# Kernel optimization log

Hardware: AMD Instinct MI355X
Metric: run time of the kernel (lower is better)

Reference implementation:

```python
import jax, jax.numpy as jnp
import numpy as np

B, TIN, E, TOUT, NMEL = 32, 512, 576, 400, 80
PRE, ARNN, DRNN, ADIM, NF, KS = 256, 1024, 1024, 128, 32, 31


def setup_inputs() -> dict:
    key = jax.random.key(0)
    ks = jax.random.split(key, 24)
    r = lambda i, sh, s=0.02: jax.random.normal(ks[i], sh, dtype=jnp.float32) * s
    return {
        'memory': jax.random.normal(ks[0], (B, TIN, E), dtype=jnp.float32) * 0.5,
        'decoder_inputs': jax.random.normal(ks[1], (B, TOUT, NMEL), dtype=jnp.float32) * 0.5,
        'prenet_W1': r(2, (PRE, NMEL)),
        'prenet_W2': r(3, (PRE, PRE)),
        'att_Wih': r(4, (4 * ARNN, PRE + E)),
        'att_Whh': r(5, (4 * ARNN, ARNN)),
        'att_bih': r(6, (4 * ARNN,)),
        'att_bhh': r(7, (4 * ARNN,)),
        'qW': r(8, (ADIM, ARNN)),
        'memW': r(9, (ADIM, E)),
        'convW': r(10, (NF, 2, KS)),
        'convb': r(11, (NF,)),
        'locW': r(12, (ADIM, NF)),
        'vW': r(13, (ADIM,)),
        'dec_Wih': r(14, (4 * DRNN, ARNN + E)),
        'dec_Whh': r(15, (4 * DRNN, DRNN)),
        'dec_bih': r(16, (4 * DRNN,)),
        'dec_bhh': r(17, (4 * DRNN,)),
        'projW': r(18, (NMEL, DRNN + E)),
        'projb': r(19, (NMEL,)),
        'gateW': r(20, (1, DRNN + E)),
        'gateb': r(21, (1,)),
        'memory_lengths': jnp.clip(jax.random.randint(ks[22], (B,), 1, TIN + 1), 16, TIN),
    }


def _lstm(x, h, c, Wih, Whh, bih, bhh):
    g = x @ Wih.T + bih + h @ Whh.T + bhh
    i, f, gg, o = jnp.split(g, 4, axis=-1)  # torch LSTMCell gate order i,f,g,o
    c = jax.nn.sigmoid(f) * c + jax.nn.sigmoid(i) * jnp.tanh(gg)
    h = jax.nn.sigmoid(o) * jnp.tanh(c)
    return h, c


def _forward(memory, decoder_inputs, prenet_W1, prenet_W2, att_Wih, att_Whh, att_bih,
             att_bhh, qW, memW, convW, convb, locW, vW, dec_Wih, dec_Whh, dec_bih,
             dec_bhh, projW, projb, gateW, gateb, memory_lengths):
    b, tin, e = memory.shape
    # go frame + teacher forcing inputs -> prenet (dropout off in deterministic eval)
    go = jnp.zeros((b, 1, NMEL), dtype=memory.dtype)
    di = jnp.concatenate([go, decoder_inputs], axis=1)          # [B, T+1, NMEL]
    x = jax.nn.relu(di @ prenet_W1.T)
    x = jax.nn.relu(x @ prenet_W2.T)                            # [B, T+1, PRE]
    xs = jnp.swapaxes(x, 0, 1)[:-1]                             # [T, B, PRE]
    pmem = memory @ memW.T                                      # [B, TIN, ADIM]
    invalid = jnp.arange(tin)[None, :] >= memory_lengths[:, None]
    pad = KS // 2

    init = (jnp.zeros((b, ARNN)), jnp.zeros((b, ARNN)),
            jnp.zeros((b, DRNN)), jnp.zeros((b, DRNN)),
            jnp.zeros((b, tin)), jnp.zeros((b, tin)),
            jnp.zeros((b, e)))

    def step(carry, xt):
        ah, ac, dh, dc, aw, awc, ctx = carry
        ci = jnp.concatenate([xt, ctx], axis=-1)
        ah, ac = _lstm(ci, ah, ac, att_Wih, att_Whh, att_bih, att_bhh)
        ah = ac  # faithful to source: dropout(attention_cell) overwrites hidden (identity in eval)
        wc = jnp.stack([aw, awc], axis=1)                       # [B, 2, TIN]
        loc = jax.lax.conv_general_dilated(
            wc, convW, (1,), [(pad, pad)],
            dimension_numbers=('NCH', 'OIH', 'NCH')) + convb[None, :, None]
        loc = jnp.swapaxes(loc, 1, 2) @ locW.T                  # [B, TIN, ADIM]
        q = (ah @ qW.T)[:, None, :]                             # [B, 1, ADIM]
        en = jnp.tanh(q + pmem + loc) @ vW                      # [B, TIN]
        en = jnp.where(invalid, -jnp.inf, en)
        aw = jax.nn.softmax(en, axis=1)
        ctx = jnp.einsum('bt,bte->be', aw, memory)
        awc = awc + aw
        d_in = jnp.concatenate([ah, ctx], axis=-1)
        dh, dc = _lstm(d_in, dh, dc, dec_Wih, dec_Whh, dec_bih, dec_bhh)
        dhc = jnp.concatenate([dh, ctx], axis=-1)
        mel = dhc @ projW.T + projb                             # [B, NMEL]
        gate = (dhc @ gateW.T + gateb)[:, 0]                    # [B]
        return (ah, ac, dh, dc, aw, awc, ctx), (mel, gate, aw)

    _, (mels, gates, aligns) = jax.lax.scan(step, init, xs)
    mel_out = jnp.swapaxes(jnp.swapaxes(mels, 0, 1), 1, 2)      # [B, NMEL, T]
    gate_out = jnp.swapaxes(gates, 0, 1)                        # [B, T]
    align_out = jnp.swapaxes(aligns, 0, 1)                      # [B, T, TIN]
    return mel_out, gate_out, align_out


def reference(memory, decoder_inputs, prenet_W1, prenet_W2, att_Wih, att_Whh, att_bih,
              att_bhh, qW, memW, convW, convb, locW, vW, dec_Wih, dec_Whh, dec_bih,
              dec_bhh, projW, projb, gateW, gateb, memory_lengths):
    return _forward(memory, decoder_inputs, prenet_W1, prenet_W2, att_Wih, att_Whh,
                    att_bih, att_bhh, qW, memW, convW, convb, locW, vW, dec_Wih,
                    dec_Whh, dec_bih, dec_bhh, projW, projb, gateW, gateb,
                    memory_lengths)
```

## Files before the change

### kernel.cpp

```cpp
#include <hip/hip_runtime.h>
#include <stdint.h>


#define NB  32
#define TI  512
#define ED  576
#define TO  400
#define NM  80
#define PR  256
#define AR  1024
#define DR  1024
#define AD  128
#define NFl 32
#define KSz 31
#define KA  1856
#define KD  2624
#define NKT_A 58
#define NKT_D 82
#define REL_IDX 320
#define MF_OFF  512

#define SCR_CWB 3584
#define SCR_ACC 4608
#define SCR_DCC 4736
#define SCR_SQ  4864
#define LDS_WA_BYTES (NKT_A*512*2)
#define LDS_WD_BYTES (NKT_D*512*2)
#define LDS_SCR_FLOATS 4992
#define LDS_TOTAL (LDS_WA_BYTES + LDS_WD_BYTES + LDS_SCR_FLOATS*4)

typedef __attribute__((ext_vector_type(8))) short bf8_t;
typedef __attribute__((ext_vector_type(4))) float f4_t;
typedef __attribute__((ext_vector_type(2))) float f2_t;
typedef unsigned long long ull;

__device__ __forceinline__ short f2bf(float f){
  union { float f; unsigned u; } v; v.f = f;
  unsigned r = v.u + 0x7fffu + ((v.u >> 16) & 1u);
  return (short)(r >> 16);
}
__device__ __forceinline__ float bf2f(short s){
  union { unsigned u; float f; } v; v.u = ((unsigned)(unsigned short)s) << 16; return v.f;
}
__device__ __forceinline__ float sigm(float x){ return 1.f / (1.f + __expf(-x)); }

__device__ __forceinline__ f4_t MFMA(bf8_t a, bf8_t b, f4_t c){
  return __builtin_amdgcn_mfma_f32_16x16x32_bf16(a, b, c, 0, 0, 0);
}

__device__ __forceinline__ float cld(const float* p){
  return __hip_atomic_load(p, __ATOMIC_RELAXED, __HIP_MEMORY_SCOPE_AGENT);
}
__device__ __forceinline__ void cst(float* p, float v){
  __hip_atomic_store(p, v, __ATOMIC_RELAXED, __HIP_MEMORY_SCOPE_AGENT);
}
__device__ __forceinline__ ull cld8(const void* p){
  return __hip_atomic_load((const ull*)p, __ATOMIC_RELAXED, __HIP_MEMORY_SCOPE_AGENT);
}
__device__ __forceinline__ void cst8(void* p, ull v){
  __hip_atomic_store((ull*)p, v, __ATOMIC_RELAXED, __HIP_MEMORY_SCOPE_AGENT);
}
__device__ __forceinline__ bf8_t cld_bf8(const short* p){
  union { bf8_t v; ull q[2]; } u;
  u.q[0] = cld8(p); u.q[1] = cld8(p + 4);
  return u.v;
}
__device__ __forceinline__ void cst_bf8(short* p, bf8_t v){
  union { bf8_t v; ull q[2]; } u; u.v = v;
  cst8(p, u.q[0]); cst8(p + 4, u.q[1]);
}

__device__ __forceinline__ bf8_t packrow(const float* p){
  f4_t a = *(const f4_t*)p;
  f4_t b = *(const f4_t*)(p + 4);
  bf8_t r;
  r[0]=f2bf(a[0]); r[1]=f2bf(a[1]); r[2]=f2bf(a[2]); r[3]=f2bf(a[3]);
  r[4]=f2bf(b[0]); r[5]=f2bf(b[1]); r[6]=f2bf(b[2]); r[7]=f2bf(b[3]);
  return r;
}
__device__ __forceinline__ bf8_t packrow_coh(const float* p){
  union { ull q; float f[2]; } u0, u1, u2, u3;
  u0.q = cld8(p); u1.q = cld8(p + 2); u2.q = cld8(p + 4); u3.q = cld8(p + 6);
  bf8_t r;
  r[0]=f2bf(u0.f[0]); r[1]=f2bf(u0.f[1]);
  r[2]=f2bf(u1.f[0]); r[3]=f2bf(u1.f[1]);
  r[4]=f2bf(u2.f[0]); r[5]=f2bf(u2.f[1]);
  r[6]=f2bf(u3.f[0]); r[7]=f2bf(u3.f[1]);
  return r;
}

struct Par {
  const float *X2, *PMEM;
  const short *WA, *WD, *WQ, *WLOC, *MEMBT, *PJW;
  const float *BSA, *BSD;
  const float *convW, *convb, *vW;
  const float *projb, *gateb;
  const int *mlen;
  float *AC, *DH, *CTX, *AW, *AWC, *EN, *QP;
  short *ABA, *ABD;
  float *out_mel, *out_gate, *out_align;
  unsigned *FLAGS;
};

__device__ __forceinline__ const float* aptr_att(const Par& p, int rp, int t, int b, int k){
  if (k < PR)      return p.X2 + ((size_t)t*NB + b)*PR + k;
  if (k < PR+ED)   return p.CTX + (size_t)rp*NB*ED + b*ED + (k - PR);
  return p.AC + (size_t)b*AR + (k - PR - ED);
}

__device__ __forceinline__ void loadD(const Par& p, int cpar, int ks, int lane,
                                      bf8_t& a0, bf8_t& a1){
  if (ks >= 32 && ks < 50){
    const int kb = ks*32 + ((lane >> 4) << 3);
    const float* c0 = p.CTX + (size_t)cpar*NB*ED + (size_t)(lane & 15)*ED + (kb - AR);
    const float* c1 = p.CTX + (size_t)cpar*NB*ED + (size_t)(16 + (lane & 15))*ED + (kb - AR);
    a0 = packrow_coh(c0);
    a1 = packrow_coh(c1);
  } else {
    a0 = cld_bf8(p.ABD + ((size_t)(0*NKT_D + ks)*64 + lane)*8);
    a1 = cld_bf8(p.ABD + ((size_t)(1*NKT_D + ks)*64 + lane)*8);
  }
}

__device__ __forceinline__ void gbar(unsigned* flags, unsigned tgt){
  __syncthreads();
  if (threadIdx.x == 0)
    __hip_atomic_store(&flags[blockIdx.x], tgt, __ATOMIC_RELAXED, __HIP_MEMORY_SCOPE_AGENT);
  if (blockIdx.x == 0){
    if (threadIdx.x < 256){
      while (__hip_atomic_load(&flags[threadIdx.x], __ATOMIC_RELAXED, __HIP_MEMORY_SCOPE_AGENT) < tgt) {}
    }
    __syncthreads();
    if (threadIdx.x == 0)
      __hip_atomic_store(&flags[REL_IDX], tgt, __ATOMIC_RELAXED, __HIP_MEMORY_SCOPE_AGENT);
  }
  if (threadIdx.x == 0){
    while (__hip_atomic_load(&flags[REL_IDX], __ATOMIC_RELAXED, __HIP_MEMORY_SCOPE_AGENT) < tgt) {}
  }
  __syncthreads();
}

__device__ __forceinline__ void sibbar(unsigned* mf, int bid, int tid, unsigned tgt){
  __syncthreads();
  if (tid == 0)
    __hip_atomic_store(&mf[bid], tgt, __ATOMIC_RELAXED, __HIP_MEMORY_SCOPE_AGENT);
  const int g = (bid >> 3) << 3;
  if (tid < 8){
    while (__hip_atomic_load(&mf[g + tid], __ATOMIC_RELAXED, __HIP_MEMORY_SCOPE_AGENT) < tgt) {}
  }
  __syncthreads();
}

__device__ __forceinline__ void reduce8(float* scr, f4_t& a0, f4_t& a1, int lane, int wv){
  if (wv > 0){
    float* slot = scr + (size_t)((wv - 1)*64 + lane)*8;
    *(f4_t*)slot       = a0;
    *(f4_t*)(slot + 4) = a1;
  }
  __syncthreads();
  if (wv == 0){
    #pragma unroll
    for (int w = 0; w < 7; ++w){
      const float* s2 = scr + (size_t)(w*64 + lane)*8;
      a0 += *(const f4_t*)s2;
      a1 += *(const f4_t*)(s2 + 4);
    }
  }
  __syncthreads();
}

__device__ __forceinline__ void dec_gates_cell(const Par& p, const short* sWD, float* scr,
                                               float* sDCc, int cpar, int bid,
                                               int lane, int wv, int tid){
  f4_t acc0 = (f4_t){0.f,0.f,0.f,0.f}, acc1 = (f4_t){0.f,0.f,0.f,0.f};
  {
    bf8_t A0[6], A1[6];
    #pragma unroll
    for (int i = 0; i < 6; ++i) loadD(p, cpar, wv + i*8, lane, A0[i], A1[i]);
    #pragma unroll
    for (int i = 0; i < 6; ++i){
      const bf8_t bw = *((const bf8_t*)sWD + (wv + i*8)*64 + lane);
      acc0 = MFMA(A0[i], bw, acc0);
      acc1 = MFMA(A1[i], bw, acc1);
    }
  }
  {
    bf8_t A0[5], A1[5];
    #pragma unroll
    for (int i = 0; i < 5; ++i){
      const int ks = wv + (i + 6)*8;
      if (ks < NKT_D) loadD(p, cpar, ks, lane, A0[i], A1[i]);
    }
    #pragma unroll
    for (int i = 0; i < 5; ++i){
      const int ks = wv + (i + 6)*8;
      if (ks < NKT_D){
        const bf8_t bw = *((const bf8_t*)sWD + ks*64 + lane);
        acc0 = MFMA(A0[i], bw, acc0);
        acc1 = MFMA(A1[i], bw, acc1);
      }
    }
  }
  reduce8(scr, acc0, acc1, lane, wv);
  float* sG = scr;
  if (wv == 0){
    const int col = lane & 15, rb2 = (lane >> 4) << 2;
    const int jp = (col & 3)*1024 + bid*4 + (col >> 2);
    const float bs = p.BSD[jp];
    #pragma unroll
    for (int r = 0; r < 4; ++r){
      sG[(rb2 + r)*16 + col]      = acc0[r] + bs;
      sG[(16 + rb2 + r)*16 + col] = acc1[r] + bs;
    }
  }
  __syncthreads();
  if (tid < 128){
    const int b = tid >> 2, ul = tid & 3;
    const float gi = sG[b*16 + ul*4 + 0];
    const float gf = sG[b*16 + ul*4 + 1];
    const float gg = sG[b*16 + ul*4 + 2];
    const float go = sG[b*16 + ul*4 + 3];
    const float c  = sigm(gf) * sDCc[tid] + sigm(gi) * tanhf(gg);
    sDCc[tid] = c;
    cst(&p.DH[(size_t)b*DR + bid*4 + ul], sigm(go) * tanhf(c));
  }
  __syncthreads();
}

__device__ void dec_proj(const Par& p, int b, int tprev, int tid, float* sIN){
  const float* ctxg = p.CTX + (size_t)(tprev & 1)*NB*ED + b*ED;
  float h0  = cld(&p.DH[(size_t)b*DR + tid]);
  float h1  = cld(&p.DH[(size_t)b*DR + 512 + tid]);
  float cx0 = cld(ctxg + tid);
  float cx1 = (tid < ED - 512) ? cld(ctxg + 512 + tid) : 0.f;
  sIN[tid] = h0; sIN[512 + tid] = h1;
  sIN[1024 + tid] = cx0;
  if (tid < ED - 512) sIN[1536 + tid] = cx1;
  if (tid < 448) sIN[1600 + tid] = 0.f;
  __syncthreads();
  const int lane = tid & 63, wv = tid >> 6;
  for (int o = wv; o < 81; o += 8){
    const short* wr = p.PJW + (size_t)o*2048 + lane*8;
    float s = 0.f;
    #pragma unroll
    for (int j = 0; j < 4; ++j){
      const bf8_t w8 = *(const bf8_t*)(wr + j*512);
      const float* v = sIN + j*512 + lane*8;
      s += v[0]*bf2f(w8[0]) + v[1]*bf2f(w8[1]) + v[2]*bf2f(w8[2]) + v[3]*bf2f(w8[3])
         + v[4]*bf2f(w8[4]) + v[5]*bf2f(w8[5]) + v[6]*bf2f(w8[6]) + v[7]*bf2f(w8[7]);
    }
    #pragma unroll
    for (int d = 32; d > 0; d >>= 1) s += __shfl_down(s, d);
    if (lane == 0){
      if (o < 80) p.out_mel[((size_t)b*NM + o)*TO + tprev] = s + p.projb[o];
      else        p.out_gate[(size_t)b*TO + tprev] = s + p.gateb[0];
    }
  }
  __syncthreads();
}

__global__ __launch_bounds__(512) void k_loop(Par p){
  const int bid = blockIdx.x, tid = threadIdx.x;
  const int lane = tid & 63, wv = tid >> 6;

  extern __shared__ char dsm[];
  short* sWA = (short*)dsm;
  short* sWD = (short*)(dsm + LDS_WA_BYTES);
  float* scr = (float*)(dsm + LDS_WA_BYTES + LDS_WD_BYTES);
  float* sACc = scr + SCR_ACC;
  float* sDCc = scr + SCR_DCC;
  unsigned* mf = p.FLAGS + MF_OFF;

  {
    if (tid < 128){ sACc[tid] = 0.f; sDCc[tid] = 0.f; }
    const bf8_t* gwa = (const bf8_t*)(p.WA + (size_t)bid*NKT_A*512);
    bf8_t* lwa = (bf8_t*)sWA;
    for (int i = tid; i < NKT_A*64; i += 512) lwa[i] = gwa[i];
    const bf8_t* gwd = (const bf8_t*)(p.WD + (size_t)bid*NKT_D*512);
    bf8_t* lwd = (bf8_t*)sWD;
    for (int i = tid; i < NKT_D*64; i += 512) lwd[i] = gwd[i];
    __syncthreads();
  }

  for (int t = 0; t < TO; ++t){
    const int wp = t & 1, rp = wp ^ 1;
    const unsigned base = (unsigned)(t * 3);

    {
      f4_t acc0 = (f4_t){0.f,0.f,0.f,0.f}, acc1 = (f4_t){0.f,0.f,0.f,0.f};
      bf8_t A0[8], A1[8];
      #pragma unroll
      for (int i = 0; i < 8; ++i){
        const int ks = wv + i*8;
        if (ks < NKT_A){
          if (t == 0 || (ks >= 8 && ks < 26)){
            const int kb = ks*32 + ((lane >> 4) << 3);
            const float* p0 = aptr_att(p, rp, t, lane & 15, kb);
            const float* p1 = aptr_att(p, rp, t, 16 + (lane & 15), kb);
            if (kb < PR){ A0[i] = packrow(p0);     A1[i] = packrow(p1);     }
            else        { A0[i] = packrow_coh(p0); A1[i] = packrow_coh(p1); }
          } else {
            A0[i] = cld_bf8(p.ABA + ((size_t)(0*NKT_A + ks)*64 + lane)*8);
            A1[i] = cld_bf8(p.ABA + ((size_t)(1*NKT_A + ks)*64 + lane)*8);
          }
        }
      }
      #pragma unroll
      for (int i = 0; i < 8; ++i){
        const int ks = wv + i*8;
        if (ks < NKT_A){
          const bf8_t bw = *((const bf8_t*)sWA + ks*64 + lane);
          acc0 = MFMA(A0[i], bw, acc0);
          acc1 = MFMA(A1[i], bw, acc1);
        }
      }
      reduce8(scr, acc0, acc1, lane, wv);
      float* sG = scr;
      if (wv == 0){
        const int col = lane & 15, rb2 = (lane >> 4) << 2;
        const int jp = (col & 3)*1024 + bid*4 + (col >> 2);
        const float bs = p.BSA[jp];
        #pragma unroll
        for (int r = 0; r < 4; ++r){
          sG[(rb2 + r)*16 + col]      = acc0[r] + bs;
          sG[(16 + rb2 + r)*16 + col] = acc1[r] + bs;
        }
      }
      __syncthreads();
      if (tid < 128){
        const int b = tid >> 2, ul = tid & 3;
        const float gi = sG[b*16 + ul*4 + 0];
        const float gf = sG[b*16 + ul*4 + 1];
        const float gg = sG[b*16 + ul*4 + 2];
        const float c  = sigm(gf) * sACc[tid] + sigm(gi) * tanhf(gg);
        sACc[tid] = c;
        cst(&p.AC[(size_t)b*AR + bid*4 + ul], c);
      }
      __syncthreads();
      if (t > 0) dec_gates_cell(p, sWD, scr, sDCc, rp, bid, lane, wv, tid);
      const int b = bid >> 3, tc = bid & 7, t0 = tc*64;
      float* sAWI = scr;
      short* sCwB = (short*)(scr + SCR_CWB);
      for (int i = tid; i < 94; i += 512){
        int g = t0 - 15 + i;
        float a = 0.f, w = 0.f;
        if (g >= 0 && g < TI){
          a = cld(&p.AW [(size_t)rp*NB*TI + b*TI + g]);
          w = cld(&p.AWC[(size_t)rp*NB*TI + b*TI + g]);
        }
        sAWI[2*i] = a; sAWI[2*i + 1] = w;
      }
      __syncthreads();
      {
        const int wvu = __builtin_amdgcn_readfirstlane(wv);
        const int f0 = wvu * 4;
        float ac4[4];
        #pragma unroll
        for (int ff = 0; ff < 4; ++ff) ac4[ff] = p.convb[f0 + ff];
        for (int k = 0; k < KSz; ++k){
          f2_t a2 = *(const f2_t*)&sAWI[2*(lane + k)];
          #pragma unroll
          for (int ff = 0; ff < 4; ++ff){
            ac4[ff] += a2[0] * p.convW[((f0+ff)*2 + 0)*KSz + k]
                     + a2[1] * p.convW[((f0+ff)*2 + 1)*KSz + k];
          }
        }
        #pragma unroll
        for (int ff = 0; ff < 4; ++ff) sCwB[lane*32 + f0 + ff] = f2bf(ac4[ff]);
      }
    }
    gbar(p.FLAGS, base + 1);

    {
      if (bid < 32){
        const int nt = bid >> 2, kc = bid & 3;
        const int kt = kc*8 + wv;
        const int kb = kt*32 + ((lane >> 4) << 3);
        bf8_t a0 = packrow_coh(p.AC + (size_t)(lane & 15)*AR + kb);
        bf8_t a1 = packrow_coh(p.AC + (size_t)(16 + (lane & 15))*AR + kb);
        const bf8_t bw = *(const bf8_t*)(p.WQ + ((size_t)(nt*32 + kt)*64 + lane)*8);
        f4_t q0 = (f4_t){0.f,0.f,0.f,0.f}, q1 = (f4_t){0.f,0.f,0.f,0.f};
        q0 = MFMA(a0, bw, q0);
        q1 = MFMA(a1, bw, q1);
        reduce8(scr, q0, q1, lane, wv);
        if (wv == 0){
          const int col = lane & 15, rb2 = (lane >> 4) << 2;
          float* qp = p.QP + (size_t)kc*NB*AD;
          #pragma unroll
          for (int r = 0; r < 4; ++r){
            cst(&qp[(rb2 + r)*AD + nt*16 + col],      q0[r]);
            cst(&qp[(16 + rb2 + r)*AD + nt*16 + col], q1[r]);
          }
        }
      }
      if (bid >= 224 && t > 0) dec_proj(p, bid - 224, t - 1, tid, scr);
    }
    gbar(p.FLAGS, base + 2);

    {
      float* sQ = scr + SCR_SQ;
      if (tid < 128){
        const int b = bid >> 3;
        sQ[tid] = cld(&p.QP[(size_t)b*AD + tid])
                + cld(&p.QP[(size_t)NB*AD + b*AD + tid])
                + cld(&p.QP[(size_t)2*NB*AD + b*AD + tid])
                + cld(&p.QP[(size_t)3*NB*AD + b*AD + tid]);
      }
      if (wv == 0 && bid < 208){
        const int r = lane & 15, koff = (lane >> 4) << 3;
        if (bid < 80){
          if (t < TO - 1){
            const int m = bid / 40, idx = bid % 40;
            const int ks = (idx < 8) ? idx : idx + 18;
            const int row = m*16 + r;
            const int k = ks*32 + koff;
            bf8_t v = (k < PR)
              ? packrow(p.X2 + ((size_t)(t+1)*NB + row)*PR + k)
              : packrow_coh(p.AC + (size_t)row*AR + (k - PR - ED));
            cst_bf8(p.ABA + ((size_t)(m*NKT_A + ks)*64 + lane)*8, v);
          }
        } else {
          const int j2 = bid - 80;
          const int m = j2 / 64, idx = j2 % 64;
          const int ks = (idx < 32) ? idx : idx + 18;
          const int row = m*16 + r;
          const int k = ks*32 + koff;
          bf8_t v = (k < AR)
            ? packrow_coh(p.AC + (size_t)row*AR + k)
            : packrow_coh(p.DH + (size_t)row*DR + (k - AR - ED));
          cst_bf8(p.ABD + ((size_t)(m*NKT_D + ks)*64 + lane)*8, v);
        }
      }
      __syncthreads();
      const int b = bid >> 3, tc = bid & 7, t0 = tc*64;
      short* sCwB = (short*)(scr + SCR_CWB);
      float* eP = scr;
      const int g = lane >> 4, li = lane & 15;
      const int d2 = wv*16 + li;
      const float vw = p.vW[d2];
      const float qd = sQ[d2];
      const bf8_t bfr = *(const bf8_t*)(p.WLOC + (size_t)(wv*64 + lane)*8);
      #pragma unroll
      for (int mt = 0; mt < 4; ++mt){
        const bf8_t afr = *(const bf8_t*)(sCwB + (mt*16 + li)*32 + (g << 3));
        f4_t c = (f4_t){0.f,0.f,0.f,0.f};
        c = MFMA(afr, bfr, c);
        #pragma unroll
        for (int r = 0; r < 4; ++r){
          const int tg = t0 + mt*16 + g*4 + r;
          const float val = c[r] + p.PMEM[((size_t)b*TI + tg)*AD + d2];
          float v = vw * tanhf(qd + val);
          v += __shfl_xor(v, 1);
          v += __shfl_xor(v, 2);
          v += __shfl_xor(v, 4);
          v += __shfl_xor(v, 8);
          if (li == 0) eP[wv*64 + mt*16 + g*4 + r] = v;
        }
      }
      __syncthreads();
      if (tid < 64){
        float e = eP[tid];
        #pragma unroll
        for (int w2 = 1; w2 < 8; ++w2) e += eP[w2*64 + tid];
        const int tg = t0 + tid;
        cst(&p.EN[b*TI + tg], (tg < p.mlen[b]) ? e : -1e30f);
      }
    }
    sibbar(mf, bid, tid, (unsigned)(t + 1));

    {
      const int b = bid >> 3, ec = bid & 7;
      float* red = scr;
      float* sp  = scr + 64;
      const float e = cld(&p.EN[b*TI + tid]);
      float m = e;
      #pragma unroll
      for (int d = 32; d > 0; d >>= 1) m = fmaxf(m, __shfl_xor(m, d));
      if (lane == 0) red[wv] = m;
      __syncthreads();
      const float M = fmaxf(fmaxf(fmaxf(red[0], red[1]), fmaxf(red[2], red[3])),
                            fmaxf(fmaxf(red[4], red[5]), fmaxf(red[6], red[7])));
      const float x = __expf(e - M);
      float z = x;
      #pragma unroll
      for (int d = 32; d > 0; d >>= 1) z += __shfl_xor(z, d);
      __syncthreads();
      if (lane == 0) red[wv] = z;
      __syncthreads();
      const float Z = red[0]+red[1]+red[2]+red[3]+red[4]+red[5]+red[6]+red[7];
      const float pv = x / Z;
      sp[tid] = pv;
      __syncthreads();
      if (ec == 0){
        cst(&p.AW [(size_t)wp*NB*TI + b*TI + tid], pv);
        cst(&p.AWC[(size_t)wp*NB*TI + b*TI + tid],
            cld(&p.AWC[(size_t)rp*NB*TI + b*TI + tid]) + pv);
        p.out_align[((size_t)b*TO + t)*TI + tid] = pv;
      }
      #pragma unroll
      for (int ii = 0; ii < 9; ++ii){
        const int e2 = ec*72 + wv*9 + ii;
        const short* row = p.MEMBT + ((size_t)b*ED + e2)*TI;
        const bf8_t w8 = *(const bf8_t*)(row + lane*8);
        const float* v = sp + lane*8;
        float a2 = v[0]*bf2f(w8[0]) + v[1]*bf2f(w8[1]) + v[2]*bf2f(w8[2]) + v[3]*bf2f(w8[3])
                 + v[4]*bf2f(w8[4]) + v[5]*bf2f(w8[5]) + v[6]*bf2f(w8[6]) + v[7]*bf2f(w8[7]);
        #pragma unroll
        for (int d = 32; d > 0; d >>= 1) a2 += __shfl_down(a2, d);
        if (lane == 0)
          cst(&p.CTX[(size_t)wp*NB*ED + b*ED + e2], a2);
      }
    }
    gbar(p.FLAGS, base + 3);
  }

  dec_gates_cell(p, sWD, scr, sDCc, (TO - 1) & 1, bid, lane, wv, tid);
  gbar(p.FLAGS, (unsigned)(TO*3 + 1));
  if (bid >= 224) dec_proj(p, bid - 224, TO - 1, tid, scr);
}

__global__ __launch_bounds__(256) void k_init(float* z, int nz,
                                              float* bsa, const float* a1, const float* a2,
                                              float* bsd, const float* d1, const float* d2){
  const int idx = blockIdx.x*256 + threadIdx.x, st = gridDim.x*256;
  const int NG = 4096;
  for (int i = idx; i < nz; i += st) z[i] = 0.f;
  for (int i = idx; i < NG; i += st){ bsa[i] = a1[i] + a2[i]; bsd[i] = d1[i] + d2[i]; }
}

__global__ __launch_bounds__(256) void k_prenet1(const float* di, const float* W1, float* X1){
  const int t = blockIdx.x, tid = threadIdx.x;
  __shared__ float sdi[NB*NM];
  for (int i = tid; i < NB*NM; i += 256){
    const int b = i / NM, k = i - b*NM;
    sdi[i] = (t == 0) ? 0.f : di[((size_t)b*TO + (t-1))*NM + k];
  }
  __syncthreads();
  float acc[NB];
  #pragma unroll
  for (int b = 0; b < NB; ++b) acc[b] = 0.f;
  const int j = tid;
  for (int k = 0; k < NM; ++k){
    const float w = W1[j*NM + k];
    #pragma unroll
    for (int b = 0; b < NB; ++b) acc[b] += sdi[b*NM + k] * w;
  }
  for (int b = 0; b < NB; ++b)
    X1[((size_t)t*NB + b)*PR + j] = fmaxf(acc[b], 0.f);
}

__global__ __launch_bounds__(256) void k_prenet2(const float* X1, const float* W2, float* X2){
  const int t = blockIdx.x, tid = threadIdx.x;
  __shared__ float sx[NB*PR];
  for (int i = tid; i < NB*PR; i += 256) sx[i] = X1[(size_t)t*NB*PR + i];
  __syncthreads();
  float acc[NB];
  #pragma unroll
  for (int b = 0; b < NB; ++b) acc[b] = 0.f;
  const int j = tid;
  for (int k = 0; k < PR; ++k){
    const float w = W2[j*PR + k];
    #pragma unroll
    for (int b = 0; b < NB; ++b) acc[b] += sx[b*PR + k] * w;
  }
  for (int b = 0; b < NB; ++b)
    X2[((size_t)t*NB + b)*PR + j] = fmaxf(acc[b], 0.f);
}

__global__ __launch_bounds__(256) void k_pmem(const float* mem, const float* memW, float* pm){
  const int b = blockIdx.x >> 3, tc = blockIdx.x & 7, tid = threadIdx.x;
  __shared__ float sW[64*AD];
  __shared__ float sM[64*65];
  const int tl = tid >> 2, dq = tid & 3;
  float acc[32];
  #pragma unroll
  for (int i = 0; i < 32; ++i) acc[i] = 0.f;
  for (int kc = 0; kc < 9; ++kc){
    __syncthreads();
    for (int i = tid; i < 64*AD; i += 256){
      const int d = i >> 6, kl = i & 63;
      sW[kl*AD + ((d + kl) & 127)] = memW[(size_t)d*ED + kc*64 + kl];
    }
    for (int i = tid; i < 64*64; i += 256){
      const int tt = i >> 6, kl = i & 63;
      sM[tt*65 + kl] = mem[((size_t)b*TI + tc*64 + tt)*ED + kc*64 + kl];
    }
    __syncthreads();
    for (int kl = 0; kl < 64; ++kl){
      const float mv = sM[tl*65 + kl];
      #pragma unroll
      for (int d2 = 0; d2 < 32; ++d2)
        acc[d2] += mv * sW[kl*AD + ((dq*32 + d2 + kl) & 127)];
    }
  }
  for (int d2 = 0; d2 < 32; ++d2)
    pm[((size_t)b*TI + tc*64 + tl)*AD + dq*32 + d2] = acc[d2];
}

__global__ __launch_bounds__(256) void k_membt(const float* mem, short* mt){
  const int b = blockIdx.x / 36, ec = blockIdx.x % 36;
  __shared__ float sT[64*17];
  for (int tc = 0; tc < 8; ++tc){
    __syncthreads();
    for (int i = threadIdx.x; i < 64*16; i += 256){
      const int tt = i >> 4, e = i & 15;
      sT[tt*17 + e] = mem[((size_t)b*TI + tc*64 + tt)*ED + ec*16 + e];
    }
    __syncthreads();
    for (int i = threadIdx.x; i < 16*64; i += 256){
      const int e = i >> 6, tt = i & 63;
      mt[((size_t)b*ED + ec*16 + e)*TI + tc*64 + tt] = f2bf(sT[tt*17 + e]);
    }
  }
}

__global__ __launch_bounds__(64) void k_swz_gate(const float* Wih, const float* Whh,
                                                 short* dst, int split, int nkt){
  const int bidx = blockIdx.x;
  const int nt = bidx / nkt, kt = bidx - nt*nkt;
  const int lane = threadIdx.x;
  const int nl = lane & 15;
  const int jp = (nl & 3)*1024 + nt*4 + (nl >> 2);
  const int k0 = kt*32 + ((lane >> 4) << 3);
  bf8_t v;
  #pragma unroll
  for (int jj = 0; jj < 8; ++jj){
    const int k = k0 + jj;
    const float f = (k < split) ? Wih[(size_t)jp*split + k]
                                : Whh[(size_t)jp*1024 + (k - split)];
    v[jj] = f2bf(f);
  }
  *(bf8_t*)(dst + (size_t)bidx*512 + lane*8) = v;
}

__global__ __launch_bounds__(64) void k_swz_q(const float* qW, short* dst){
  const int bidx = blockIdx.x;
  const int nt = bidx >> 5, kt = bidx & 31;
  const int lane = threadIdx.x;
  const int d = nt*16 + (lane & 15);
  const int k0 = kt*32 + ((lane >> 4) << 3);
  bf8_t v;
  #pragma unroll
  for (int jj = 0; jj < 8; ++jj) v[jj] = f2bf(qW[(size_t)d*AR + k0 + jj]);
  *(bf8_t*)(dst + (size_t)bidx*512 + lane*8) = v;
}

__global__ __launch_bounds__(64) void k_swz_loc(const float* locW, short* dst){
  const int nt = blockIdx.x;
  const int lane = threadIdx.x;
  const int d = nt*16 + (lane & 15);
  const int f0 = (lane >> 4) << 3;
  bf8_t v;
  #pragma unroll
  for (int jj = 0; jj < 8; ++jj) v[jj] = f2bf(locW[d*NFl + f0 + jj]);
  *(bf8_t*)(dst + (size_t)(nt*64 + lane)*8) = v;
}

__global__ __launch_bounds__(256) void k_swz_proj(const float* projW, const float* gateW,
                                                  short* dst){
  const int o = blockIdx.x;
  const float* src = (o < 80) ? (projW + (size_t)o*1600) : gateW;
  for (int k = threadIdx.x; k < 2048; k += 256)
    dst[(size_t)o*2048 + k] = (k < 1600) ? f2bf(src[k]) : (short)0;
}

extern "C" void kernel_launch(void* const* d_in, const int* in_sizes, int n_in,
                              void* d_out, int out_size, void* d_ws, size_t ws_size,
                              hipStream_t stream){
  const float* mem    = (const float*)d_in[0];
  const float* dec_in = (const float*)d_in[1];
  const float* pW1    = (const float*)d_in[2];
  const float* pW2    = (const float*)d_in[3];
  const float* aWih   = (const float*)d_in[4];
  const float* aWhh   = (const float*)d_in[5];
  const float* aBih   = (const float*)d_in[6];
  const float* aBhh   = (const float*)d_in[7];
  const float* qW     = (const float*)d_in[8];
  const float* memW   = (const float*)d_in[9];
  const float* convW  = (const float*)d_in[10];
  const float* convb  = (const float*)d_in[11];
  const float* locW   = (const float*)d_in[12];
  const float* vW     = (const float*)d_in[13];
  const float* dWih   = (const float*)d_in[14];
  const float* dWhh   = (const float*)d_in[15];
  const float* dBih   = (const float*)d_in[16];
  const float* dBhh   = (const float*)d_in[17];
  const float* projW  = (const float*)d_in[18];
  const float* projb  = (const float*)d_in[19];
  const float* gateW  = (const float*)d_in[20];
  const float* gateb  = (const float*)d_in[21];
  const int*   mlen   = (const int*)d_in[22];
  (void)in_sizes; (void)n_in; (void)out_size; (void)ws_size;

  char* basep = (char*)d_ws;
  size_t off = 0;
  auto carve = [&](size_t bytes) -> char* {
    char* r = basep + off;
    off = (off + bytes + 255) & ~(size_t)255;
    return r;
  };
  const int NG = 4096;
  short* WA    = (short*)carve((size_t)NG*KA*2);
  short* WD    = (short*)carve((size_t)NG*KD*2);
  short* WQ    = (short*)carve((size_t)AD*AR*2);
  short* WLOC  = (short*)carve((size_t)AD*NFl*2);
  short* MEMBT = (short*)carve((size_t)NB*TI*ED*2);
  short* PJW   = (short*)carve((size_t)81*2048*2);
  float* X1    = (float*)carve((size_t)TO*NB*PR*4);
  float* X2    = (float*)carve((size_t)TO*NB*PR*4);
  float* PMEM  = (float*)carve((size_t)NB*TI*AD*4);
  float* BSA   = (float*)carve((size_t)NG*4);
  float* BSD   = (float*)carve((size_t)NG*4);
  short* ABA   = (short*)carve((size_t)2*NKT_A*512*2);
  short* ABD   = (short*)carve((size_t)2*NKT_D*512*2);
  float* AC    = (float*)carve((size_t)NB*AR*4);
  float* DH    = (float*)carve((size_t)NB*DR*4);
  float* CTX   = (float*)carve((size_t)2*NB*ED*4);
  float* AW    = (float*)carve((size_t)2*NB*TI*4);
  float* AWC   = (float*)carve((size_t)2*NB*TI*4);
  float* EN    = (float*)carve((size_t)NB*TI*4);
  float* QP    = (float*)carve((size_t)4*NB*AD*4);
  unsigned* FLAGS = (unsigned*)carve(4096);
  const int nz = (int)((((char*)FLAGS + 4096) - (char*)AC) / 4);

  float* out_mel   = (float*)d_out;
  float* out_gate  = out_mel + (size_t)NB*NM*TO;
  float* out_align = out_gate + (size_t)NB*TO;

  k_init   <<<dim3(512), dim3(256), 0, stream>>>(AC, nz, BSA, aBih, aBhh, BSD, dBih, dBhh);
  k_prenet1<<<dim3(TO),  dim3(256), 0, stream>>>(dec_in, pW1, X1);
  k_prenet2<<<dim3(TO),  dim3(256), 0, stream>>>(X1, pW2, X2);
  k_pmem   <<<dim3(256), dim3(256), 0, stream>>>(mem, memW, PMEM);
  k_membt  <<<dim3(NB*36), dim3(256), 0, stream>>>(mem, MEMBT);
  k_swz_gate<<<dim3(256*NKT_A), dim3(64), 0, stream>>>(aWih, aWhh, WA, 832, NKT_A);
  k_swz_gate<<<dim3(256*NKT_D), dim3(64), 0, stream>>>(dWih, dWhh, WD, 1600, NKT_D);
  k_swz_q  <<<dim3(256), dim3(64), 0, stream>>>(qW, WQ);
  k_swz_loc<<<dim3(8),   dim3(64), 0, stream>>>(locW, WLOC);
  k_swz_proj<<<dim3(81), dim3(256), 0, stream>>>(projW, gateW, PJW);

  Par p;
  p.X2 = X2; p.PMEM = PMEM;
  p.WA = WA; p.WD = WD; p.WQ = WQ; p.WLOC = WLOC; p.MEMBT = MEMBT; p.PJW = PJW;
  p.BSA = BSA; p.BSD = BSD;
  p.convW = convW; p.convb = convb; p.vW = vW;
  p.projb = projb; p.gateb = gateb;
  p.mlen = mlen;
  p.AC = AC; p.DH = DH; p.CTX = CTX;
  p.AW = AW; p.AWC = AWC; p.EN = EN; p.QP = QP;
  p.ABA = ABA; p.ABD = ABD;
  p.out_mel = out_mel; p.out_gate = out_gate; p.out_align = out_align;
  p.FLAGS = FLAGS;

  (void)hipFuncSetAttribute((const void*)k_loop,
                            hipFuncAttributeMaxDynamicSharedMemorySize, LDS_TOTAL);
  k_loop<<<dim3(256), dim3(512), LDS_TOTAL, stream>>>(p);
}
```

Measured before the change: 32.43 ms.

## Hoist precomputable LSTM gate MFMAs before barrier and repartition barrier phases

Splits the attention and decoder LSTM gate GEMMs so the parts whose operands are already packed (ABA/ABD buffers) run before the first grid barrier, leaving only the context-dependent k-tiles on the critical path after it. The bf16 operand packing work moves from the post-barrier phase into idle blocks of the query-projection phase, and the barrier count per step is reshuffled. LDS scratch layouts for the cross-wave reduction, the projection input and the softmax probabilities are padded (stride 65/72) to avoid bank conflicts. This adds complexity and extra scratch, and the final-step decoder cell now needs its own extra grid barrier.

```diff
diff --git a/kernel.cpp b/kernel.cpp
--- a/kernel.cpp
+++ b/kernel.cpp
@@ -20,18 +20,17 @@
 #define REL_IDX 320
 #define MF_OFF  512
 
-#define SCR_CWB 3584
-#define SCR_ACC 4608
-#define SCR_DCC 4736
-#define SCR_SQ  4864
+#define SCR_CWB 3640
+#define SCR_ACC 4664
+#define SCR_DCC 4792
+#define SCR_SQ  4920
 #define LDS_WA_BYTES (NKT_A*512*2)
 #define LDS_WD_BYTES (NKT_D*512*2)
-#define LDS_SCR_FLOATS 4992
+#define LDS_SCR_FLOATS 5048
 #define LDS_TOTAL (LDS_WA_BYTES + LDS_WD_BYTES + LDS_SCR_FLOATS*4)
 
 typedef __attribute__((ext_vector_type(8))) short bf8_t;
 typedef __attribute__((ext_vector_type(4))) float f4_t;
-typedef __attribute__((ext_vector_type(2))) float f2_t;
 typedef unsigned long long ull;
 
 __device__ __forceinline__ short f2bf(float f){
@@ -108,18 +107,21 @@
   return p.AC + (size_t)b*AR + (k - PR - ED);
 }
 
-__device__ __forceinline__ void loadD(const Par& p, int cpar, int ks, int lane,
-                                      bf8_t& a0, bf8_t& a1){
-  if (ks >= 32 && ks < 50){
-    const int kb = ks*32 + ((lane >> 4) << 3);
-    const float* c0 = p.CTX + (size_t)cpar*NB*ED + (size_t)(lane & 15)*ED + (kb - AR);
-    const float* c1 = p.CTX + (size_t)cpar*NB*ED + (size_t)(16 + (lane & 15))*ED + (kb - AR);
-    a0 = packrow_coh(c0);
-    a1 = packrow_coh(c1);
-  } else {
-    a0 = cld_bf8(p.ABD + ((size_t)(0*NKT_D + ks)*64 + lane)*8);
-    a1 = cld_bf8(p.ABD + ((size_t)(1*NKT_D + ks)*64 + lane)*8);
-  }
+__device__ __forceinline__ void ldABA(const Par& p, int ks, int lane, bf8_t& a0, bf8_t& a1){
+  a0 = cld_bf8(p.ABA + ((size_t)(0*NKT_A + ks)*64 + lane)*8);
+  a1 = cld_bf8(p.ABA + ((size_t)(1*NKT_A + ks)*64 + lane)*8);
+}
+__device__ __forceinline__ void ldABD(const Par& p, int ks, int lane, bf8_t& a0, bf8_t& a1){
+  a0 = cld_bf8(p.ABD + ((size_t)(0*NKT_D + ks)*64 + lane)*8);
+  a1 = cld_bf8(p.ABD + ((size_t)(1*NKT_D + ks)*64 + lane)*8);
+}
+__device__ __forceinline__ void ldCTXfr(const Par& p, int cpar, int ks, int sub, int lane,
+                                        bf8_t& a0, bf8_t& a1){
+  const int kb = ks*32 + ((lane >> 4) << 3);
+  const float* c0 = p.CTX + (size_t)cpar*NB*ED + (size_t)(lane & 15)*ED + (kb - sub);
+  const float* c1 = p.CTX + (size_t)cpar*NB*ED + (size_t)(16 + (lane & 15))*ED + (kb - sub);
+  a0 = packrow_coh(c0);
+  a1 = packrow_coh(c1);
 }
 
 __device__ __forceinline__ void gbar(unsigned* flags, unsigned tgt){
@@ -153,55 +155,88 @@
 
 __device__ __forceinline__ void reduce8(float* scr, f4_t& a0, f4_t& a1, int lane, int wv){
   if (wv > 0){
-    float* slot = scr + (size_t)((wv - 1)*64 + lane)*8;
-    *(f4_t*)slot       = a0;
-    *(f4_t*)(slot + 4) = a1;
+    float* base = scr + (size_t)(wv - 1)*520;
+    #pragma unroll
+    for (int e = 0; e < 4; ++e) base[e*65 + lane] = a0[e];
+    #pragma unroll
+    for (int e = 0; e < 4; ++e) base[(4 + e)*65 + lane] = a1[e];
   }
   __syncthreads();
   if (wv == 0){
     #pragma unroll
     for (int w = 0; w < 7; ++w){
-      const float* s2 = scr + (size_t)(w*64 + lane)*8;
-      a0 += *(const f4_t*)s2;
-      a1 += *(const f4_t*)(s2 + 4);
-    }
-  }
-  __syncthreads();
-}
-
-__device__ __forceinline__ void dec_gates_cell(const Par& p, const short* sWD, float* scr,
-                                               float* sDCc, int cpar, int bid,
-                                               int lane, int wv, int tid){
-  f4_t acc0 = (f4_t){0.f,0.f,0.f,0.f}, acc1 = (f4_t){0.f,0.f,0.f,0.f};
+      const float* base = scr + (size_t)w*520;
+      #pragma unroll
+      for (int e = 0; e < 4; ++e) a0[e] += base[e*65 + lane];
+      #pragma unroll
+      for (int e = 0; e < 4; ++e) a1[e] += base[(4 + e)*65 + lane];
+    }
+  }
+  __syncthreads();
+}
+
+__device__ __forceinline__ void dec_prep(const Par& p, const short* sWD,
+                                         int lane, int wv, f4_t& d0, f4_t& d1){
   {
-    bf8_t A0[6], A1[6];
-    #pragma unroll
-    for (int i = 0; i < 6; ++i) loadD(p, cpar, wv + i*8, lane, A0[i], A1[i]);
-    #pragma unroll
-    for (int i = 0; i < 6; ++i){
-      const bf8_t bw = *((const bf8_t*)sWD + (wv + i*8)*64 + lane);
-      acc0 = MFMA(A0[i], bw, acc0);
-      acc1 = MFMA(A1[i], bw, acc1);
+    bf8_t A0a,A1a,A0b,A1b,A0c,A1c,A0d,A1d,A0e,A1e;
+    const bool e_ok = (wv >= 2);
+    ldABD(p, wv +  0, lane, A0a, A1a);
+    ldABD(p, wv +  8, lane, A0b, A1b);
+    ldABD(p, wv + 16, lane, A0c, A1c);
+    ldABD(p, wv + 24, lane, A0d, A1d);
+    if (e_ok) ldABD(p, wv + 48, lane, A0e, A1e);
+    d0 = MFMA(A0a, *((const bf8_t*)sWD + (wv+ 0)*64 + lane), d0);
+    d1 = MFMA(A1a, *((const bf8_t*)sWD + (wv+ 0)*64 + lane), d1);
+    d0 = MFMA(A0b, *((const bf8_t*)sWD + (wv+ 8)*64 + lane), d0);
+    d1 = MFMA(A1b, *((const bf8_t*)sWD + (wv+ 8)*64 + lane), d1);
+    d0 = MFMA(A0c, *((const bf8_t*)sWD + (wv+16)*64 + lane), d0);
+    d1 = MFMA(A1c, *((const bf8_t*)sWD + (wv+16)*64 + lane), d1);
+    d0 = MFMA(A0d, *((const bf8_t*)sWD + (wv+24)*64 + lane), d0);
+    d1 = MFMA(A1d, *((const bf8_t*)sWD + (wv+24)*64 + lane), d1);
+    if (e_ok){
+      d0 = MFMA(A0e, *((const bf8_t*)sWD + (wv+48)*64 + lane), d0);
+      d1 = MFMA(A1e, *((const bf8_t*)sWD + (wv+48)*64 + lane), d1);
     }
   }
   {
-    bf8_t A0[5], A1[5];
-    #pragma unroll
-    for (int i = 0; i < 5; ++i){
-      const int ks = wv + (i + 6)*8;
-      if (ks < NKT_D) loadD(p, cpar, ks, lane, A0[i], A1[i]);
-    }
-    #pragma unroll
-    for (int i = 0; i < 5; ++i){
-      const int ks = wv + (i + 6)*8;
-      if (ks < NKT_D){
-        const bf8_t bw = *((const bf8_t*)sWD + ks*64 + lane);
-        acc0 = MFMA(A0[i], bw, acc0);
-        acc1 = MFMA(A1[i], bw, acc1);
-      }
-    }
-  }
-  reduce8(scr, acc0, acc1, lane, wv);
+    bf8_t B0a,B1a,B0b,B1b,B0c,B1c,B0d,B1d;
+    const bool d_ok = (wv < 2);
+    ldABD(p, wv + 56, lane, B0a, B1a);
+    ldABD(p, wv + 64, lane, B0b, B1b);
+    ldABD(p, wv + 72, lane, B0c, B1c);
+    if (d_ok) ldABD(p, wv + 80, lane, B0d, B1d);
+    d0 = MFMA(B0a, *((const bf8_t*)sWD + (wv+56)*64 + lane), d0);
+    d1 = MFMA(B1a, *((const bf8_t*)sWD + (wv+56)*64 + lane), d1);
+    d0 = MFMA(B0b, *((const bf8_t*)sWD + (wv+64)*64 + lane), d0);
+    d1 = MFMA(B1b, *((const bf8_t*)sWD + (wv+64)*64 + lane), d1);
+    d0 = MFMA(B0c, *((const bf8_t*)sWD + (wv+72)*64 + lane), d0);
+    d1 = MFMA(B1c, *((const bf8_t*)sWD + (wv+72)*64 + lane), d1);
+    if (d_ok){
+      d0 = MFMA(B0d, *((const bf8_t*)sWD + (wv+80)*64 + lane), d0);
+      d1 = MFMA(B1d, *((const bf8_t*)sWD + (wv+80)*64 + lane), d1);
+    }
+  }
+}
+
+__device__ __forceinline__ void dec_finish(const Par& p, const short* sWD, float* scr,
+                                           float* sDCc, int cpar, int bid,
+                                           int lane, int wv, int tid, f4_t d0, f4_t d1){
+  {
+    bf8_t C0a,C1a,C0b,C1b,C0c,C1c;
+    const bool c_ok = (wv < 2);
+    ldCTXfr(p, cpar, wv + 32, AR, lane, C0a, C1a);
+    ldCTXfr(p, cpar, wv + 40, AR, lane, C0b, C1b);
+    if (c_ok) ldCTXfr(p, cpar, wv + 48, AR, lane, C0c, C1c);
+    d0 = MFMA(C0a, *((const bf8_t*)sWD + (wv+32)*64 + lane), d0);
+    d1 = MFMA(C1a, *((const bf8_t*)sWD + (wv+32)*64 + lane), d1);
+    d0 = MFMA(C0b, *((const bf8_t*)sWD + (wv+40)*64 + lane), d0);
+    d1 = MFMA(C1b, *((const bf8_t*)sWD + (wv+40)*64 + lane), d1);
+    if (c_ok){
+      d0 = MFMA(C0c, *((const bf8_t*)sWD + (wv+48)*64 + lane), d0);
+      d1 = MFMA(C1c, *((const bf8_t*)sWD + (wv+48)*64 + lane), d1);
+    }
+  }
+  reduce8(scr, d0, d1, lane, wv);
   float* sG = scr;
   if (wv == 0){
     const int col = lane & 15, rb2 = (lane >> 4) << 2;
@@ -209,8 +244,8 @@
     const float bs = p.BSD[jp];
     #pragma unroll
     for (int r = 0; r < 4; ++r){
-      sG[(rb2 + r)*16 + col]      = acc0[r] + bs;
-      sG[(16 + rb2 + r)*16 + col] = acc1[r] + bs;
+      sG[(rb2 + r)*16 + col]      = d0[r] + bs;
+      sG[(16 + rb2 + r)*16 + col] = d1[r] + bs;
     }
   }
   __syncthreads();
@@ -227,16 +262,20 @@
   __syncthreads();
 }
 
+__device__ __forceinline__ int soa_in(int u){
+  return (u >> 9)*520 + (u & 7)*65 + ((u >> 3) & 63);
+}
 __device__ void dec_proj(const Par& p, int b, int tprev, int tid, float* sIN){
   const float* ctxg = p.CTX + (size_t)(tprev & 1)*NB*ED + b*ED;
   float h0  = cld(&p.DH[(size_t)b*DR + tid]);
   float h1  = cld(&p.DH[(size_t)b*DR + 512 + tid]);
   float cx0 = cld(ctxg + tid);
-  float cx1 = (tid < ED - 512) ? cld(ctxg + 512 + tid) : 0.f;
-  sIN[tid] = h0; sIN[512 + tid] = h1;
-  sIN[1024 + tid] = cx0;
-  if (tid < ED - 512) sIN[1536 + tid] = cx1;
-  if (tid < 448) sIN[1600 + tid] = 0.f;
+  float cx1 = (tid < 64) ? cld(ctxg + 512 + tid) : 0.f;
+  sIN[soa_in(tid)]        = h0;
+  sIN[soa_in(512 + tid)]  = h1;
+  sIN[soa_in(1024 + tid)] = cx0;
+  if (tid < 64)  sIN[soa_in(1536 + tid)] = cx1;
+  if (tid < 448) sIN[soa_in(1600 + tid)] = 0.f;
   __syncthreads();
   const int lane = tid & 63, wv = tid >> 6;
   for (int o = wv; o < 81; o += 8){
@@ -245,9 +284,11 @@
     #pragma unroll
     for (int j = 0; j < 4; ++j){
       const bf8_t w8 = *(const bf8_t*)(wr + j*512);
-      const float* v = sIN + j*512 + lane*8;
-      s += v[0]*bf2f(w8[0]) + v[1]*bf2f(w8[1]) + v[2]*bf2f(w8[2]) + v[3]*bf2f(w8[3])
-         + v[4]*bf2f(w8[4]) + v[5]*bf2f(w8[5]) + v[6]*bf2f(w8[6]) + v[7]*bf2f(w8[7]);
+      const float* base = sIN + j*520 + lane;
+      s += base[0*65]*bf2f(w8[0]) + base[1*65]*bf2f(w8[1])
+         + base[2*65]*bf2f(w8[2]) + base[3*65]*bf2f(w8[3])
+         + base[4*65]*bf2f(w8[4]) + base[5*65]*bf2f(w8[5])
+         + base[6*65]*bf2f(w8[6]) + base[7*65]*bf2f(w8[7]);
     }
     #pragma unroll
     for (int d = 32; d > 0; d >>= 1) s += __shfl_down(s, d);
@@ -286,35 +327,80 @@
     const int wp = t & 1, rp = wp ^ 1;
     const unsigned base = (unsigned)(t * 3);
 
+    f4_t aA0 = (f4_t){0.f,0.f,0.f,0.f}, aA1 = (f4_t){0.f,0.f,0.f,0.f};
+    f4_t aD0 = (f4_t){0.f,0.f,0.f,0.f}, aD1 = (f4_t){0.f,0.f,0.f,0.f};
+
+    if (t > 0){
+      {
+        bf8_t A0a,A1a,A0d,A1d,A0e,A1e,A0f,A1f,A0g,A1g,A0h,A1h;
+        const bool d_ok = (wv >= 2);
+        const bool h_ok = (wv < 2);
+        ldABA(p, wv +  0, lane, A0a, A1a);
+        if (d_ok) ldABA(p, wv + 24, lane, A0d, A1d);
+        ldABA(p, wv + 32, lane, A0e, A1e);
+        ldABA(p, wv + 40, lane, A0f, A1f);
+        ldABA(p, wv + 48, lane, A0g, A1g);
+        if (h_ok) ldABA(p, wv + 56, lane, A0h, A1h);
+        aA0 = MFMA(A0a, *((const bf8_t*)sWA + (wv+ 0)*64 + lane), aA0);
+        aA1 = MFMA(A1a, *((const bf8_t*)sWA + (wv+ 0)*64 + lane), aA1);
+        if (d_ok){
+          aA0 = MFMA(A0d, *((const bf8_t*)sWA + (wv+24)*64 + lane), aA0);
+          aA1 = MFMA(A1d, *((const bf8_t*)sWA + (wv+24)*64 + lane), aA1);
+        }
+        aA0 = MFMA(A0e, *((const bf8_t*)sWA + (wv+32)*64 + lane), aA0);
+        aA1 = MFMA(A1e, *((const bf8_t*)sWA + (wv+32)*64 + lane), aA1);
+        aA0 = MFMA(A0f, *((const bf8_t*)sWA + (wv+40)*64 + lane), aA0);
+        aA1 = MFMA(A1f, *((const bf8_t*)sWA + (wv+40)*64 + lane), aA1);
+        aA0 = MFMA(A0g, *((const bf8_t*)sWA + (wv+48)*64 + lane), aA0);
+        aA1 = MFMA(A1g, *((const bf8_t*)sWA + (wv+48)*64 + lane), aA1);
+        if (h_ok){
+          aA0 = MFMA(A0h, *((const bf8_t*)sWA + (wv+56)*64 + lane), aA0);
+          aA1 = MFMA(A1h, *((const bf8_t*)sWA + (wv+56)*64 + lane), aA1);
+        }
+      }
+      dec_prep(p, sWD, lane, wv, aD0, aD1);
+    }
+    gbar(p.FLAGS, base + 1);
+
     {
-      f4_t acc0 = (f4_t){0.f,0.f,0.f,0.f}, acc1 = (f4_t){0.f,0.f,0.f,0.f};
-      bf8_t A0[8], A1[8];
-      #pragma unroll
-      for (int i = 0; i < 8; ++i){
-        const int ks = wv + i*8;
-        if (ks < NKT_A){
-          if (t == 0 || (ks >= 8 && ks < 26)){
+      if (t == 0){
+        bf8_t A0[8], A1v[8];
+        #pragma unroll
+        for (int i = 0; i < 8; ++i){
+          const int ks = wv + i*8;
+          if (ks < NKT_A){
             const int kb = ks*32 + ((lane >> 4) << 3);
             const float* p0 = aptr_att(p, rp, t, lane & 15, kb);
             const float* p1 = aptr_att(p, rp, t, 16 + (lane & 15), kb);
-            if (kb < PR){ A0[i] = packrow(p0);     A1[i] = packrow(p1);     }
-            else        { A0[i] = packrow_coh(p0); A1[i] = packrow_coh(p1); }
-          } else {
-            A0[i] = cld_bf8(p.ABA + ((size_t)(0*NKT_A + ks)*64 + lane)*8);
-            A1[i] = cld_bf8(p.ABA + ((size_t)(1*NKT_A + ks)*64 + lane)*8);
+            if (kb < PR){ A0[i] = packrow(p0);     A1v[i] = packrow(p1);     }
+            else        { A0[i] = packrow_coh(p0); A1v[i] = packrow_coh(p1); }
           }
         }
-      }
-      #pragma unroll
-      for (int i = 0; i < 8; ++i){
-        const int ks = wv + i*8;
-        if (ks < NKT_A){
-          const bf8_t bw = *((const bf8_t*)sWA + ks*64 + lane);
-          acc0 = MFMA(A0[i], bw, acc0);
-          acc1 = MFMA(A1[i], bw, acc1);
-        }
-      }
-      reduce8(scr, acc0, acc1, lane, wv);
+        #pragma unroll
+        for (int i = 0; i < 8; ++i){
+          const int ks = wv + i*8;
+          if (ks < NKT_A){
+            const bf8_t bw = *((const bf8_t*)sWA + ks*64 + lane);
+            aA0 = MFMA(A0[i], bw, aA0);
+            aA1 = MFMA(A1v[i], bw, aA1);
+          }
+        }
+      } else {
+        bf8_t C0a,C1a,C0b,C1b,C0c,C1c;
+        const bool c_ok = (wv < 2);
+        ldCTXfr(p, rp, wv +  8, PR, lane, C0a, C1a);
+        ldCTXfr(p, rp, wv + 16, PR, lane, C0b, C1b);
+        if (c_ok) ldCTXfr(p, rp, wv + 24, PR, lane, C0c, C1c);
+        aA0 = MFMA(C0a, *((const bf8_t*)sWA + (wv+ 8)*64 + lane), aA0);
+        aA1 = MFMA(C1a, *((const bf8_t*)sWA + (wv+ 8)*64 + lane), aA1);
+        aA0 = MFMA(C0b, *((const bf8_t*)sWA + (wv+16)*64 + lane), aA0);
+        aA1 = MFMA(C1b, *((const bf8_t*)sWA + (wv+16)*64 + lane), aA1);
+        if (c_ok){
+          aA0 = MFMA(C0c, *((const bf8_t*)sWA + (wv+24)*64 + lane), aA0);
+          aA1 = MFMA(C1c, *((const bf8_t*)sWA + (wv+24)*64 + lane), aA1);
+        }
+      }
+      reduce8(scr, aA0, aA1, lane, wv);
       float* sG = scr;
       if (wv == 0){
         const int col = lane & 15, rb2 = (lane >> 4) << 2;
@@ -322,8 +408,8 @@
         const float bs = p.BSA[jp];
         #pragma unroll
         for (int r = 0; r < 4; ++r){
-          sG[(rb2 + r)*16 + col]      = acc0[r] + bs;
-          sG[(16 + rb2 + r)*16 + col] = acc1[r] + bs;
+          sG[(rb2 + r)*16 + col]      = aA0[r] + bs;
+          sG[(16 + rb2 + r)*16 + col] = aA1[r] + bs;
         }
       }
       __syncthreads();
@@ -337,7 +423,7 @@
         cst(&p.AC[(size_t)b*AR + bid*4 + ul], c);
       }
       __syncthreads();
-      if (t > 0) dec_gates_cell(p, sWD, scr, sDCc, rp, bid, lane, wv, tid);
+      if (t > 0) dec_finish(p, sWD, scr, sDCc, rp, bid, lane, wv, tid, aD0, aD1);
       const int b = bid >> 3, tc = bid & 7, t0 = tc*64;
       float* sAWI = scr;
       short* sCwB = (short*)(scr + SCR_CWB);
@@ -348,7 +434,7 @@
           a = cld(&p.AW [(size_t)rp*NB*TI + b*TI + g]);
           w = cld(&p.AWC[(size_t)rp*NB*TI + b*TI + g]);
         }
-        sAWI[2*i] = a; sAWI[2*i + 1] = w;
+        sAWI[3*i] = a; sAWI[3*i + 1] = w;
       }
       __syncthreads();
       {
@@ -358,18 +444,19 @@
         #pragma unroll
         for (int ff = 0; ff < 4; ++ff) ac4[ff] = p.convb[f0 + ff];
         for (int k = 0; k < KSz; ++k){
-          f2_t a2 = *(const f2_t*)&sAWI[2*(lane + k)];
+          const float av = sAWI[3*(lane + k)];
+          const float wcv = sAWI[3*(lane + k) + 1];
           #pragma unroll
           for (int ff = 0; ff < 4; ++ff){
-            ac4[ff] += a2[0] * p.convW[((f0+ff)*2 + 0)*KSz + k]
-                     + a2[1] * p.convW[((f0+ff)*2 + 1)*KSz + k];
+            ac4[ff] += av  * p.convW[((f0+ff)*2 + 0)*KSz + k]
+                     + wcv * p.convW[((f0+ff)*2 + 1)*KSz + k];
           }
         }
         #pragma unroll
         for (int ff = 0; ff < 4; ++ff) sCwB[lane*32 + f0 + ff] = f2bf(ac4[ff]);
       }
     }
-    gbar(p.FLAGS, base + 1);
+    gbar(p.FLAGS, base + 2);
 
     {
       if (bid < 32){
@@ -392,10 +479,40 @@
             cst(&qp[(16 + rb2 + r)*AD + nt*16 + col], q1[r]);
           }
         }
-      }
-      if (bid >= 224 && t > 0) dec_proj(p, bid - 224, t - 1, tid, scr);
-    }
-    gbar(p.FLAGS, base + 2);
+      } else if (bid >= 224){
+        if (t > 0) dec_proj(p, bid - 224, t - 1, tid, scr);
+      } else {
+        int job = -1;
+        if (wv == 0) job = bid - 32;
+        else if (wv == 1 && bid < 48) job = 192 + (bid - 32);
+        if (job >= 0){
+          const int r = lane & 15, koff = (lane >> 4) << 3;
+          if (job < 80){
+            if (t < TO - 1){
+              const int m = job / 40, idx = job % 40;
+              const int ks = (idx < 8) ? idx : idx + 18;
+              const int row = m*16 + r;
+              const int k = ks*32 + koff;
+              bf8_t v = (k < PR)
+                ? packrow(p.X2 + ((size_t)(t+1)*NB + row)*PR + k)
+                : packrow_coh(p.AC + (size_t)row*AR + (k - PR - ED));
+              cst_bf8(p.ABA + ((size_t)(m*NKT_A + ks)*64 + lane)*8, v);
+            }
+          } else {
+            const int j2 = job - 80;
+            const int m = j2 / 64, idx = j2 % 64;
+            const int ks = (idx < 32) ? idx : idx + 18;
+            const int row = m*16 + r;
+            const int k = ks*32 + koff;
+            bf8_t v = (k < AR)
+              ? packrow_coh(p.AC + (size_t)row*AR + k)
+              : packrow_coh(p.DH + (size_t)row*DR + (k - AR - ED));
+            cst_bf8(p.ABD + ((size_t)(m*NKT_D + ks)*64 + lane)*8, v);
+          }
+        }
+      }
+    }
+    gbar(p.FLAGS, base + 3);
 
     {
       float* sQ = scr + SCR_SQ;
@@ -405,31 +522,6 @@
                 + cld(&p.QP[(size_t)NB*AD + b*AD + tid])
                 + cld(&p.QP[(size_t)2*NB*AD + b*AD + tid])
                 + cld(&p.QP[(size_t)3*NB*AD + b*AD + tid]);
-      }
-      if (wv == 0 && bid < 208){
-        const int r = lane & 15, koff = (lane >> 4) << 3;
-        if (bid < 80){
-          if (t < TO - 1){
-            const int m = bid / 40, idx = bid % 40;
-            const int ks = (idx < 8) ? idx : idx + 18;
-            const int row = m*16 + r;
-            const int k = ks*32 + koff;
-            bf8_t v = (k < PR)
-              ? packrow(p.X2 + ((size_t)(t+1)*NB + row)*PR + k)
-              : packrow_coh(p.AC + (size_t)row*AR + (k - PR - ED));
-            cst_bf8(p.ABA + ((size_t)(m*NKT_A + ks)*64 + lane)*8, v);
-          }
-        } else {
-          const int j2 = bid - 80;
-          const int m = j2 / 64, idx = j2 % 64;
-          const int ks = (idx < 32) ? idx : idx + 18;
-          const int row = m*16 + r;
-          const int k = ks*32 + koff;
-          bf8_t v = (k < AR)
-            ? packrow_coh(p.AC + (size_t)row*AR + k)
-            : packrow_coh(p.DH + (size_t)row*DR + (k - AR - ED));
-          cst_bf8(p.ABD + ((size_t)(m*NKT_D + ks)*64 + lane)*8, v);
-        }
       }
       __syncthreads();
       const int b = bid >> 3, tc = bid & 7, t0 = tc*64;
@@ -470,8 +562,8 @@
 
     {
       const int b = bid >> 3, ec = bid & 7;
-      float* red = scr;
-      float* sp  = scr + 64;
+      float* spS = scr;
+      float* red = scr + 576;
       const float e = cld(&p.EN[b*TI + tid]);
       float m = e;
       #pragma unroll
@@ -489,33 +581,38 @@
       __syncthreads();
       const float Z = red[0]+red[1]+red[2]+red[3]+red[4]+red[5]+red[6]+red[7];
       const float pv = x / Z;
-      sp[tid] = pv;
-      __syncthreads();
+      spS[(tid & 7)*72 + (tid >> 3)] = pv;
       if (ec == 0){
         cst(&p.AW [(size_t)wp*NB*TI + b*TI + tid], pv);
         cst(&p.AWC[(size_t)wp*NB*TI + b*TI + tid],
             cld(&p.AWC[(size_t)rp*NB*TI + b*TI + tid]) + pv);
         p.out_align[((size_t)b*TO + t)*TI + tid] = pv;
       }
+      __syncthreads();
       #pragma unroll
       for (int ii = 0; ii < 9; ++ii){
         const int e2 = ec*72 + wv*9 + ii;
         const short* row = p.MEMBT + ((size_t)b*ED + e2)*TI;
         const bf8_t w8 = *(const bf8_t*)(row + lane*8);
-        const float* v = sp + lane*8;
-        float a2 = v[0]*bf2f(w8[0]) + v[1]*bf2f(w8[1]) + v[2]*bf2f(w8[2]) + v[3]*bf2f(w8[3])
-                 + v[4]*bf2f(w8[4]) + v[5]*bf2f(w8[5]) + v[6]*bf2f(w8[6]) + v[7]*bf2f(w8[7]);
+        float a2 = spS[0*72+lane]*bf2f(w8[0]) + spS[1*72+lane]*bf2f(w8[1])
+                 + spS[2*72+lane]*bf2f(w8[2]) + spS[3*72+lane]*bf2f(w8[3])
+                 + spS[4*72+lane]*bf2f(w8[4]) + spS[5*72+lane]*bf2f(w8[5])
+                 + spS[6*72+lane]*bf2f(w8[6]) + spS[7*72+lane]*bf2f(w8[7]);
         #pragma unroll
         for (int d = 32; d > 0; d >>= 1) a2 += __shfl_down(a2, d);
         if (lane == 0)
           cst(&p.CTX[(size_t)wp*NB*ED + b*ED + e2], a2);
       }
     }
-    gbar(p.FLAGS, base + 3);
-  }
-
-  dec_gates_cell(p, sWD, scr, sDCc, (TO - 1) & 1, bid, lane, wv, tid);
+  }
+
   gbar(p.FLAGS, (unsigned)(TO*3 + 1));
+  {
+    f4_t d0 = (f4_t){0.f,0.f,0.f,0.f}, d1 = (f4_t){0.f,0.f,0.f,0.f};
+    dec_prep(p, sWD, lane, wv, d0, d1);
+    dec_finish(p, sWD, scr, sDCc, (TO - 1) & 1, bid, lane, wv, tid, d0, d1);
+  }
+  gbar(p.FLAGS, (unsigned)(TO*3 + 2));
   if (bid >= 224) dec_proj(p, bid - 224, TO - 1, tid, scr);
 }
 
```

After: 32.76 ms. Within noise of the previous version (+1.0%).
